# Kernel tuning notes

Hardware: AMD Instinct MI355X
Metric: run time of the kernel (lower is better)

## Reference

```python
import jax, jax.numpy as jnp
import numpy as np

B, N, D = 32, 128, 1024


def _euclid_cost(a, b):
    # a: [N, D], b: [N, D] -> [N, N] Euclidean distances (torch.cdist p=2)
    a = a.astype(np.float64)
    b = b.astype(np.float64)
    sq = (a * a).sum(-1)[:, None] + (b * b).sum(-1)[None, :] - 2.0 * (a @ b.T)
    return np.sqrt(np.maximum(sq, 0.0))


def _hungarian(cost):
    """Exact LAP via shortest augmenting path (Kuhn-Munkres with potentials).
    Returns col_for_row: row i is matched to column col_for_row[i].
    Equivalent to scipy.optimize.linear_sum_assignment on a square matrix
    (row_ind == arange(N))."""
    n = cost.shape[0]
    INF = 1e18
    c = cost.astype(np.float64)
    u = np.zeros(n + 1)
    v = np.zeros(n + 1)
    p = np.zeros(n + 1, dtype=np.int64)   # p[j] = row matched to column j (1-based)
    way = np.zeros(n + 1, dtype=np.int64)
    for i in range(1, n + 1):
        p[0] = i
        j0 = 0
        minv = np.full(n + 1, INF)
        used = np.zeros(n + 1, dtype=bool)
        while True:
            used[j0] = True
            i0 = p[j0]
            free = ~used[1:]
            cand = c[i0 - 1] - u[i0] - v[1:]
            better = free & (cand < minv[1:])
            idx = np.nonzero(better)[0]
            minv[idx + 1] = cand[idx]
            way[idx + 1] = j0
            free_j = np.nonzero(free)[0] + 1
            j1 = free_j[np.argmin(minv[free_j])]
            delta = minv[j1]
            u[p[used]] += delta
            v[used] -= delta
            minv[~used] -= delta
            j0 = j1
            if p[j0] == 0:
                break
        while j0:
            j1 = way[j0]
            p[j0] = p[j1]
            j0 = j1
    col_for_row = np.zeros(n, dtype=np.int64)
    for j in range(1, n + 1):
        col_for_row[p[j] - 1] = j - 1
    return col_for_row


def _match(pred_nodes, target_nodes):
    # Host-side exact bipartite matching (mirrors the .cpu() + scipy solve;
    # non-differentiable, indices treated as constants like torch's detach()).
    pn = np.asarray(jax.device_get(pred_nodes))
    tn = np.asarray(jax.device_get(target_nodes))
    cols = [_hungarian(_euclid_cost(pn[b], tn[b])) for b in range(pn.shape[0])]
    return jnp.asarray(np.stack(cols))  # [B, N] int64


def setup_inputs() -> dict:
    key = jax.random.key(0)
    k1, k2, k3, k4 = jax.random.split(key, 4)
    return {
        "pred_nodes": jax.random.normal(k1, (B, N, D), dtype=jnp.float32),
        "target_nodes": jax.random.normal(k2, (B, N, D), dtype=jnp.float32),
        "pred_adj": jax.random.normal(k3, (B, N, N), dtype=jnp.float32),
        "target_adj": jax.random.normal(k4, (B, N, N), dtype=jnp.float32),
    }


def reference(pred_nodes, target_nodes, pred_adj, target_adj):
    col = _match(pred_nodes, target_nodes)  # [B, N]; row_ind is identity
    # matched target nodes: target_nodes[b][col_ind]
    tn_m = jnp.take_along_axis(target_nodes, col[:, :, None], axis=1)  # [B, N, D]
    # nn.MSELoss() = mean over elements per sample; losses summed over batch
    node_loss = jnp.mean((pred_nodes - tn_m) ** 2, axis=(1, 2)).sum()
    # target_adj[b][col_ind][:, col_ind]; pred_adj row_ind gather is identity
    ta_m = jnp.take_along_axis(target_adj, col[:, :, None], axis=1)
    ta_m = jnp.take_along_axis(ta_m, col[:, None, :], axis=2)  # [B, N, N]
    edge_loss = jnp.mean((pred_adj - ta_m) ** 2, axis=(1, 2)).sum()
    return node_loss, edge_loss
```

## Files before the change

kernel.cpp:

```cpp
#include <hip/hip_runtime.h>
#include <hip/hip_bf16.h>
#include <math.h>

#define BB 32
#define NN 128
#define DD 1024
#define INF64 1e30

__global__ __launch_bounds__(64) void cost_kernel(const float* __restrict__ pred,
                                                  const float* __restrict__ tgt,
                                                  double* __restrict__ cost) {
  extern __shared__ double a_s[];
  __shared__ double red_s[64];
  __shared__ double na_s[8];
  int s = blockIdx.x;
  int r8 = s & 7;
  int m = s >> 3;
  int t = m & 15;
  int q = m >> 4;
  int b = 8 * q + r8;
  int it = t << 3;
  const float* Ab = pred + ((size_t)b * NN + it) * DD;
  const float* Bb = tgt + (size_t)b * NN * DD;
  const int lane = threadIdx.x;
  for (int tdx = lane; tdx < 8 * DD / 4; tdx += 64) {
    float4 v = ((const float4*)Ab)[tdx];
    double2* d = (double2*)&a_s[(size_t)tdx * 4];
    d[0] = double2{(double)v.x, (double)v.y};
    d[1] = double2{(double)v.z, (double)v.w};
  }
  __syncthreads();
  {
    int r = lane >> 3, o = lane & 7;
    const double* ar = a_s + (size_t)r * DD;
    double sum = 0.0;
    for (int k = o; k < DD; k += 8) { double x = ar[k]; sum += x * x; }
    red_s[lane] = sum;
  }
  __syncthreads();
  if (lane < 8) {
    double sum = 0.0;
#pragma unroll
    for (int mm = 0; mm < 8; mm++) sum += red_s[lane * 8 + mm];
    na_s[lane] = sum;
  }
  __syncthreads();
  const float4* brow0 = (const float4*)(Bb + (size_t)lane * DD);
  const float4* brow1 = (const float4*)(Bb + (size_t)(lane + 64) * DD);
  double acc0[8], acc1[8];
#pragma unroll
  for (int r = 0; r < 8; r++) { acc0[r] = 0.0; acc1[r] = 0.0; }
  double nb0 = 0.0, nb1 = 0.0;
  for (int k4 = 0; k4 < DD / 4; k4++) {
    float4 b0 = brow0[k4];
    float4 b1 = brow1[k4];
    double d00 = (double)b0.x, d01 = (double)b0.y, d02 = (double)b0.z, d03 = (double)b0.w;
    double d10 = (double)b1.x, d11 = (double)b1.y, d12 = (double)b1.z, d13 = (double)b1.w;
    nb0 += d00 * d00 + d01 * d01 + d02 * d02 + d03 * d03;
    nb1 += d10 * d10 + d11 * d11 + d12 * d12 + d13 * d13;
#pragma unroll
    for (int r = 0; r < 8; r++) {
      const double2* ap = (const double2*)(a_s + (size_t)r * DD + (size_t)k4 * 4);
      double2 x = ap[0];
      double2 y = ap[1];
      acc0[r] += x.x * d00 + x.y * d01 + y.x * d02 + y.y * d03;
      acc1[r] += x.x * d10 + x.y * d11 + y.x * d12 + y.y * d13;
    }
  }
#pragma unroll
  for (int r = 0; r < 8; r++) {
    double sq0 = na_s[r] + nb0 - 2.0 * acc0[r];
    double sq1 = na_s[r] + nb1 - 2.0 * acc1[r];
    size_t base = (((size_t)b * NN) + it + r) * NN;
    cost[base + lane] = sqrt(fmax(sq0, 0.0));
    cost[base + lane + 64] = sqrt(fmax(sq1, 0.0));
  }
}

union f64u { double d; unsigned int i[2]; };

__device__ __forceinline__ double readlane_f64(double x, int lane) {
  f64u u; u.d = x;
  f64u v;
  v.i[0] = (unsigned)__builtin_amdgcn_readlane((int)u.i[0], lane);
  v.i[1] = (unsigned)__builtin_amdgcn_readlane((int)u.i[1], lane);
  return v.d;
}

__device__ __forceinline__ double readpair_f64(double a, double b, int idx) {
  int l = (idx - 1) & 63;
  double ra = readlane_f64(a, l);
  double rb = readlane_f64(b, l);
  return ((idx - 1) >> 6) ? rb : ra;
}

__device__ __forceinline__ int readpair_i32(int a, int b, int idx) {
  int l = (idx - 1) & 63;
  int ra = __builtin_amdgcn_readlane(a, l);
  int rb = __builtin_amdgcn_readlane(b, l);
  return ((idx - 1) >> 6) ? rb : ra;
}

__device__ __forceinline__ double pack_key(double m, int idx) {
  unsigned long long bits = __double_as_longlong(fmax(m, 0.0));
  bits = (bits & ~127ull) | (unsigned long long)idx;
  return __longlong_as_double(bits);
}

#define DPP_MIN_STEP(r, CTRL)                                                        \
  do {                                                                               \
    f64u _t; _t.d = (r);                                                             \
    f64u _s;                                                                         \
    _s.i[0] = (unsigned)__builtin_amdgcn_update_dpp((int)_t.i[0], (int)_t.i[0],      \
                                                    (CTRL), 0xF, 0xF, false);        \
    _s.i[1] = (unsigned)__builtin_amdgcn_update_dpp((int)_t.i[1], (int)_t.i[1],      \
                                                    (CTRL), 0xF, 0xF, false);        \
    (r) = fmin((r), _s.d);                                                           \
  } while (0)

#define DPP_MIN_CHAIN(r)          \
  do {                            \
    DPP_MIN_STEP(r, 0x111);       \
    DPP_MIN_STEP(r, 0x112);       \
    DPP_MIN_STEP(r, 0x114);       \
    DPP_MIN_STEP(r, 0x118);       \
    DPP_MIN_STEP(r, 0x142);       \
    DPP_MIN_STEP(r, 0x143);       \
  } while (0)

__global__ __launch_bounds__(64) void hungarian_kernel(const double* __restrict__ cost,
                                                       int* __restrict__ colfor) {
  extern __shared__ double lds[];
  const int b = blockIdx.x;
  const double* C = cost + (size_t)b * NN * NN;
  const int lane = threadIdx.x;
  const int jA = lane + 1;
  const int jB = lane + 65;

  {
    const double2* src = (const double2*)C;
    double2* dst = (double2*)lds;
#pragma unroll 8
    for (int t = lane; t < NN * NN / 2; t += 64) dst[t] = src[t];
  }
  __syncthreads();

  double vA = INF64, vB = INF64;
  int argA = 0, argB = 0;
#pragma unroll 4
  for (int i = 0; i < NN; i++) {
    double cA = lds[(size_t)i * NN + lane];
    double cB = lds[(size_t)i * NN + lane + 64];
    if (cA < vA) { vA = cA; argA = i + 1; }
    if (cB < vB) { vB = cB; argB = i + 1; }
  }

  unsigned long long asgLo = 0ull, asgHi = 0ull;
  int pA = 0, pB = 0;
  for (int j = 1; j <= NN; j++) {
    int ar = readpair_i32(argA, argB, j);
    bool freeRow = (ar <= 64) ? !((asgLo >> (ar - 1)) & 1ull)
                              : !((asgHi >> (ar - 65)) & 1ull);
    if (freeRow) {
      if (ar <= 64) asgLo |= 1ull << (ar - 1); else asgHi |= 1ull << (ar - 65);
      if (j == jA) pA = ar;
      if (j == jB) pB = ar;
    }
  }

  double uA = 0.0, uB = 0.0;

  for (int i = 1; i <= NN; i++) {
    bool seeded = (i <= 64) ? ((asgLo >> (i - 1)) & 1ull)
                            : ((asgHi >> (i - 65)) & 1ull);
    if (seeded) continue;

    double minvA = INF64, minvB = INF64;
    int wayA = 0, wayB = 0;
    int usedA = 0, usedB = 0;
    unsigned long long usedRowLo = 0ull, usedRowHi = 0ull;
    int j0 = 0;
    int i0 = i;
    int jfin;
    while (true) {
      usedA |= (j0 == jA);
      usedB |= (j0 == jB);
      if (i0 <= 64) usedRowLo |= 1ull << (i0 - 1); else usedRowHi |= 1ull << (i0 - 65);
      double u_i0 = readpair_f64(uA, uB, i0);
      const double* crow = lds + (size_t)(i0 - 1) * NN;
      double cA = crow[lane];
      double cB = crow[lane + 64];
      double candA = cA - u_i0 - vA;
      double candB = cB - u_i0 - vB;
      if (!usedA && candA < minvA) { minvA = candA; wayA = j0; }
      if (!usedB && candB < minvB) { minvB = candB; wayB = j0; }
      double kA = pack_key(usedA ? INF64 : minvA, lane);
      double kB = pack_key(usedB ? INF64 : minvB, lane + 64);
      double r = fmin(kA, kB);
      DPP_MIN_CHAIN(r);
      double rmin = readlane_f64(r, 63);
      unsigned long long bits = __double_as_longlong(rmin);
      int j1 = (int)(bits & 127ull) + 1;
      double delta = __longlong_as_double((long long)(bits & ~127ull));
      if ((usedRowLo >> lane) & 1ull) uA += delta;
      if ((usedRowHi >> lane) & 1ull) uB += delta;
      if (usedA) vA -= delta; else minvA -= delta;
      if (usedB) vB -= delta; else minvB -= delta;
      int pj1 = readpair_i32(pA, pB, j1);
      j0 = j1;
      if (pj1 == 0) { jfin = j1; break; }
      i0 = pj1;
    }
    int j = jfin;
    while (j) {
      int wj = readpair_i32(wayA, wayB, j);
      int pn = (wj == 0) ? i : readpair_i32(pA, pB, wj);
      if (j == jA) pA = pn;
      if (j == jB) pB = pn;
      j = wj;
    }
  }
  colfor[b * NN + (pA - 1)] = jA - 1;
  colfor[b * NN + (pB - 1)] = jB - 1;
}

__global__ __launch_bounds__(256) void node_loss_kernel(const float* __restrict__ pred,
                                                        const float* __restrict__ tgt,
                                                        const int* __restrict__ col,
                                                        double* __restrict__ partial) {
  const size_t total = (size_t)BB * NN * (DD / 4);
  double s = 0.0;
  for (size_t idx = (size_t)blockIdx.x * blockDim.x + threadIdx.x; idx < total;
       idx += (size_t)gridDim.x * blockDim.x) {
    size_t k4 = idx & (DD / 4 - 1);
    size_t bi = idx / (DD / 4);
    int i = (int)(bi & (NN - 1));
    int b = (int)(bi >> 7);
    int c = col[b * NN + i];
    float4 pv = ((const float4*)pred)[idx];
    float4 tv = ((const float4*)(tgt + ((size_t)b * NN + c) * DD))[k4];
    float d0 = pv.x - tv.x, d1 = pv.y - tv.y, d2 = pv.z - tv.z, d3 = pv.w - tv.w;
    s += (double)d0 * d0 + (double)d1 * d1 + (double)d2 * d2 + (double)d3 * d3;
  }
  __shared__ double red[256];
  red[threadIdx.x] = s;
  __syncthreads();
  for (int off = 128; off > 0; off >>= 1) {
    if (threadIdx.x < off) red[threadIdx.x] += red[threadIdx.x + off];
    __syncthreads();
  }
  if (threadIdx.x == 0) partial[blockIdx.x] = red[0];
}

__global__ __launch_bounds__(256) void edge_loss_kernel(const float* __restrict__ padj,
                                                        const float* __restrict__ tadj,
                                                        const int* __restrict__ col,
                                                        double* __restrict__ partial) {
  const size_t total = (size_t)BB * NN * NN;
  double s = 0.0;
  for (size_t idx = (size_t)blockIdx.x * blockDim.x + threadIdx.x; idx < total;
       idx += (size_t)gridDim.x * blockDim.x) {
    int j = (int)(idx & (NN - 1));
    size_t bi = idx >> 7;
    int i = (int)(bi & (NN - 1));
    int b = (int)(bi >> 7);
    int ci = col[b * NN + i];
    int cj = col[b * NN + j];
    float diff = padj[idx] - tadj[((size_t)b * NN + ci) * NN + cj];
    s += (double)diff * (double)diff;
  }
  __shared__ double red[256];
  red[threadIdx.x] = s;
  __syncthreads();
  for (int off = 128; off > 0; off >>= 1) {
    if (threadIdx.x < off) red[threadIdx.x] += red[threadIdx.x + off];
    __syncthreads();
  }
  if (threadIdx.x == 0) partial[blockIdx.x] = red[0];
}

__global__ __launch_bounds__(256) void finalize_kernel(const double* __restrict__ nodeP, int nNode,
                                                       const double* __restrict__ edgeP, int nEdge,
                                                       float* __restrict__ out) {
  __shared__ double red[256];
  double s = 0.0;
  for (int t = threadIdx.x; t < nNode; t += 256) s += nodeP[t];
  red[threadIdx.x] = s;
  __syncthreads();
  for (int off = 128; off > 0; off >>= 1) {
    if (threadIdx.x < off) red[threadIdx.x] += red[threadIdx.x + off];
    __syncthreads();
  }
  double nodeSum = red[0];
  __syncthreads();
  s = 0.0;
  for (int t = threadIdx.x; t < nEdge; t += 256) s += edgeP[t];
  red[threadIdx.x] = s;
  __syncthreads();
  for (int off = 128; off > 0; off >>= 1) {
    if (threadIdx.x < off) red[threadIdx.x] += red[threadIdx.x + off];
    __syncthreads();
  }
  if (threadIdx.x == 0) {
    out[0] = (float)(nodeSum / (double)(NN * DD));
    out[1] = (float)(red[0] / (double)(NN * NN));
  }
}

extern "C" void kernel_launch(void* const* d_in, const int* in_sizes, int n_in,
                              void* d_out, int out_size, void* d_ws, size_t ws_size,
                              hipStream_t stream) {
  const float* pred_nodes   = (const float*)d_in[0];
  const float* target_nodes = (const float*)d_in[1];
  const float* pred_adj     = (const float*)d_in[2];
  const float* target_adj   = (const float*)d_in[3];
  float* out = (float*)d_out;

  char* ws = (char*)d_ws;
  double* cost = (double*)ws;
  size_t off = (size_t)BB * NN * NN * sizeof(double);
  int* col = (int*)(ws + off);
  off += (size_t)BB * NN * sizeof(int);
  double* nodeP = (double*)(ws + off);
  double* edgeP = nodeP + 512;

  cost_kernel<<<BB * 16, 64, 65536, stream>>>(pred_nodes, target_nodes, cost);
  hungarian_kernel<<<BB, 64, 131072, stream>>>(cost, col);
  node_loss_kernel<<<512, 256, 0, stream>>>(pred_nodes, target_nodes, col, nodeP);
  edge_loss_kernel<<<128, 256, 0, stream>>>(pred_adj, target_adj, col, edgeP);
  finalize_kernel<<<1, 256, 0, stream>>>(nodeP, 512, edgeP, 128, out);
}
```

Baseline: 810.7 us.

## Add row-reduction seeding to Hungarian and derive node loss from cost matrix

Adds a second greedy initialisation pass in the Hungarian kernel. For each unassigned row it computes the reduced-cost minimum with a DPP wave reduction, sets the row potential, and assigns the row if that column is still free, so fewer rows need full augmenting-path searches. It also drops the separate node_loss kernel and computes the node loss from the squared matched Euclidean costs already held in LDS, which avoids re-reading both 16 MB node tensors. The squared cost comes from a distance expanded as norms minus a dot product, so it can differ slightly from the direct sum of squared differences, and the finalize kernel now sums 4096 partials instead of 512.

```diff
diff --git a/kernel.cpp b/kernel.cpp
--- a/kernel.cpp
+++ b/kernel.cpp
@@ -129,7 +129,8 @@
   } while (0)
 
 __global__ __launch_bounds__(64) void hungarian_kernel(const double* __restrict__ cost,
-                                                       int* __restrict__ colfor) {
+                                                       int* __restrict__ colfor,
+                                                       double* __restrict__ nodeC) {
   extern __shared__ double lds[];
   const int b = blockIdx.x;
   const double* C = cost + (size_t)b * NN * NN;
@@ -169,6 +170,35 @@
   }
 
   double uA = 0.0, uB = 0.0;
+
+  {
+    unsigned long long fLo = __ballot(pA == 0);
+    unsigned long long fHi = __ballot(pB == 0);
+    unsigned long long itLo = ~asgLo, itHi = ~asgHi;
+    while ((itLo | itHi) != 0ull) {
+      int i = itLo ? (__builtin_ctzll(itLo) + 1) : (__builtin_ctzll(itHi) + 65);
+      if (i <= 64) itLo &= ~(1ull << (i - 1)); else itHi &= ~(1ull << (i - 65));
+      const double* crow = lds + (size_t)(i - 1) * NN;
+      double candA = crow[lane] - vA;
+      double candB = crow[lane + 64] - vB;
+      double r = fmin(pack_key(candA, lane), pack_key(candB, lane + 64));
+      DPP_MIN_CHAIN(r);
+      unsigned long long bits = __double_as_longlong(readlane_f64(r, 63));
+      int jstar = (int)(bits & 127ull) + 1;
+      double mi = readpair_f64(candA, candB, jstar);
+      if (i <= 64) { if (lane == i - 1) uA = mi; }
+      else         { if (lane == i - 65) uB = mi; }
+      bool jfree = (jstar <= 64) ? ((fLo >> (jstar - 1)) & 1ull)
+                                 : ((fHi >> (jstar - 65)) & 1ull);
+      if (jfree) {
+        if (jstar == jA) pA = i;
+        if (jstar == jB) pB = i;
+        if (jstar <= 64) fLo &= ~(1ull << (jstar - 1));
+        else             fHi &= ~(1ull << (jstar - 65));
+        if (i <= 64) asgLo |= 1ull << (i - 1); else asgHi |= 1ull << (i - 65);
+      }
+    }
+  }
 
   for (int i = 1; i <= NN; i++) {
     bool seeded = (i <= 64) ? ((asgLo >> (i - 1)) & 1ull)
@@ -222,34 +252,12 @@
   }
   colfor[b * NN + (pA - 1)] = jA - 1;
   colfor[b * NN + (pB - 1)] = jB - 1;
-}
-
-__global__ __launch_bounds__(256) void node_loss_kernel(const float* __restrict__ pred,
-                                                        const float* __restrict__ tgt,
-                                                        const int* __restrict__ col,
-                                                        double* __restrict__ partial) {
-  const size_t total = (size_t)BB * NN * (DD / 4);
-  double s = 0.0;
-  for (size_t idx = (size_t)blockIdx.x * blockDim.x + threadIdx.x; idx < total;
-       idx += (size_t)gridDim.x * blockDim.x) {
-    size_t k4 = idx & (DD / 4 - 1);
-    size_t bi = idx / (DD / 4);
-    int i = (int)(bi & (NN - 1));
-    int b = (int)(bi >> 7);
-    int c = col[b * NN + i];
-    float4 pv = ((const float4*)pred)[idx];
-    float4 tv = ((const float4*)(tgt + ((size_t)b * NN + c) * DD))[k4];
-    float d0 = pv.x - tv.x, d1 = pv.y - tv.y, d2 = pv.z - tv.z, d3 = pv.w - tv.w;
-    s += (double)d0 * d0 + (double)d1 * d1 + (double)d2 * d2 + (double)d3 * d3;
-  }
-  __shared__ double red[256];
-  red[threadIdx.x] = s;
-  __syncthreads();
-  for (int off = 128; off > 0; off >>= 1) {
-    if (threadIdx.x < off) red[threadIdx.x] += red[threadIdx.x + off];
-    __syncthreads();
-  }
-  if (threadIdx.x == 0) partial[blockIdx.x] = red[0];
+  {
+    double c1 = lds[(size_t)(pA - 1) * NN + lane];
+    double c2 = lds[(size_t)(pB - 1) * NN + lane + 64];
+    nodeC[b * NN + lane] = c1 * c1;
+    nodeC[b * NN + lane + 64] = c2 * c2;
+  }
 }
 
 __global__ __launch_bounds__(256) void edge_loss_kernel(const float* __restrict__ padj,
@@ -321,12 +329,12 @@
   size_t off = (size_t)BB * NN * NN * sizeof(double);
   int* col = (int*)(ws + off);
   off += (size_t)BB * NN * sizeof(int);
-  double* nodeP = (double*)(ws + off);
-  double* edgeP = nodeP + 512;
+  double* nodeC = (double*)(ws + off);
+  off += (size_t)BB * NN * sizeof(double);
+  double* edgeP = (double*)(ws + off);
 
   cost_kernel<<<BB * 16, 64, 65536, stream>>>(pred_nodes, target_nodes, cost);
-  hungarian_kernel<<<BB, 64, 131072, stream>>>(cost, col);
-  node_loss_kernel<<<512, 256, 0, stream>>>(pred_nodes, target_nodes, col, nodeP);
+  hungarian_kernel<<<BB, 64, 131072, stream>>>(cost, col, nodeC);
   edge_loss_kernel<<<128, 256, 0, stream>>>(pred_adj, target_adj, col, edgeP);
-  finalize_kernel<<<1, 256, 0, stream>>>(nodeP, 512, edgeP, 128, out);
-}
+  finalize_kernel<<<1, 256, 0, stream>>>(nodeC, BB * NN, edgeP, 128, out);
+}
```

After: 793.0 us (median of 2 runs). -2.2%, faster.
